# Kernel tuning notes

Measured on AMD Instinct MI355X. Metric: run time of the kernel, lower is better.

The kernel has to match this reference:

```python
import jax, jax.numpy as jnp
import numpy as np

KH, KW = 3, 3  # window_size[1], window_size[2]
SH, SW = 1, 1  # strides
FILTERS = 64


def _extract_patches(x, kh, kw, sh, sw):
    # TF tf.image.extract_patches ordering: depth = (row, col, channel), channel fastest.
    B, H, W, C = x.shape
    Ho = (H - kh) // sh + 1
    Wo = (W - kw) // sw + 1
    # stack kh*kw shifted views -> (B, Ho, Wo, kh*kw, C)
    views = [x[:, i:i + (Ho - 1) * sh + 1:sh, j:j + (Wo - 1) * sw + 1:sw, :]
             for i in range(kh) for j in range(kw)]
    patches = jnp.stack(views, axis=3)
    return patches.reshape(B, Ho, Wo, kh * kw * C)


def setup_inputs() -> dict:
    key = jax.random.key(0)
    k1, k2 = jax.random.split(key)
    B, H, W, C = 8, 32, 32, 32
    K = KH * KW * C  # 288
    x = jax.random.normal(k1, (B, H, W, C), dtype=jnp.float32)
    w = jax.random.normal(k2, (1, 1, 1, K, FILTERS), dtype=jnp.float32) * 0.05
    bias = jnp.zeros((FILTERS,), dtype=jnp.float32)
    return {"x": x, "w": w, "bias": bias}


def reference(x, w, bias):
    # patches: (B, Ho, Wo, K)
    patches = _extract_patches(x, KH, KW, SH, SW)
    # broadcast add: (B, Ho, Wo, K, F)
    s = patches[..., None] + w
    # tropical max-plus minus min-plus over the patch axis, plus bias
    return jnp.max(s, axis=3) - jnp.min(s, axis=3) + bias
```

## Files before the change

kernel.cpp:

```cpp
#include <hip/hip_runtime.h>
#include <math.h>


#define PIX 6

__global__ __launch_bounds__(64) void trop_kernel(
    const float* __restrict__ x,
    const float* __restrict__ w,
    const float* __restrict__ bias,
    float* __restrict__ out)
{
    const int lane = threadIdx.x;
    const int gid  = blockIdx.x;
    const int chunk = gid % 5;
    const int rowid = gid / 5;
    const int ho = rowid % 30;
    const int b  = rowid / 30;
    const int wo0 = chunk * PIX;

    const float* xbase = x + (((b * 32 + ho) * 32) + wo0) * 32;

    float amax[PIX], amin[PIX];
#pragma unroll
    for (int p = 0; p < PIX; ++p) {
        amax[p] = -INFINITY;
        amin[p] =  INFINITY;
    }

#pragma unroll
    for (int dydx = 0; dydx < 9; ++dydx) {
        const int dy = dydx / 3;
        const int dx = dydx % 3;
        const float* xp = xbase + (dy * 32 + dx) * 32;
        const float* wp = w + dydx * 32 * 64 + lane;

        for (int c = 0; c < 32; c += 4) {
            const float w0 = wp[(c + 0) * 64];
            const float w1 = wp[(c + 1) * 64];
            const float w2 = wp[(c + 2) * 64];
            const float w3 = wp[(c + 3) * 64];
#pragma unroll
            for (int p = 0; p < PIX; ++p) {
                const float4 xv = *(const float4*)(xp + p * 32 + c);
                const float s0 = xv.x + w0;
                const float s1 = xv.y + w1;
                const float s2 = xv.z + w2;
                const float s3 = xv.w + w3;
                amax[p] = fmaxf(fmaxf(fmaxf(fmaxf(amax[p], s0), s1), s2), s3);
                amin[p] = fminf(fminf(fminf(fminf(amin[p], s0), s1), s2), s3);
            }
        }
    }

    const float bv = bias[lane];
    float* op = out + (((b * 30 + ho) * 30) + wo0) * 64 + lane;
#pragma unroll
    for (int p = 0; p < PIX; ++p)
        op[p * 64] = amax[p] - amin[p] + bv;
}

extern "C" void kernel_launch(void* const* d_in, const int* in_sizes, int n_in,
                              void* d_out, int out_size, void* d_ws, size_t ws_size,
                              hipStream_t stream) {
    const float* x    = (const float*)d_in[0];
    const float* w    = (const float*)d_in[1];
    const float* bias = (const float*)d_in[2];
    float* out = (float*)d_out;

    trop_kernel<<<dim3(1200), dim3(64), 0, stream>>>(x, w, bias, out);
}
```

Measured before the change: 82.23 us.

## Stage weights in double-buffered LDS and shrink per-wave pixel tile

Weights for each 3x3 tap are cooperatively loaded into a double-buffered shared-memory tile by a 256-thread block. The next tap is prefetched into registers while the current one is used, so lanes no longer issue global loads for weights. The pixel tile per wave drops from 6 to 2, which raises the wave count (900 blocks of 4 waves) to improve latency hiding. The cost is a barrier per tap, extra LDS traffic, and less reuse of each weight value across pixels.

```diff
diff --git a/kernel.cpp b/kernel.cpp
--- a/kernel.cpp
+++ b/kernel.cpp
@@ -2,46 +2,68 @@
 #include <math.h>
 
 
-#define PIX 6
+#define PIX 2
+#define TPB 256
 
-__global__ __launch_bounds__(64) void trop_kernel(
+__global__ __launch_bounds__(TPB) void trop_kernel(
     const float* __restrict__ x,
     const float* __restrict__ w,
     const float* __restrict__ bias,
     float* __restrict__ out)
 {
-    const int lane = threadIdx.x;
-    const int gid  = blockIdx.x;
-    const int chunk = gid % 5;
-    const int rowid = gid / 5;
-    const int ho = rowid % 30;
-    const int b  = rowid / 30;
-    const int wo0 = chunk * PIX;
+    __shared__ float wlds[2][32 * 64];
 
-    const float* xbase = x + (((b * 32 + ho) * 32) + wo0) * 32;
+    const int tid  = threadIdx.x;
+    const int lane = tid & 63;
+    const int wv   = tid >> 6;
+
+    const int pix0 = blockIdx.x * (4 * PIX) + wv * PIX;
+
+    const float* xp[PIX];
+#pragma unroll
+    for (int p = 0; p < PIX; ++p) {
+        const int pid = pix0 + p;
+        const int wo = pid % 30;
+        const int t  = pid / 30;
+        const int ho = t % 30;
+        const int b  = t / 30;
+        xp[p] = x + (((b * 32 + ho) * 32) + wo) * 32;
+    }
 
     float amax[PIX], amin[PIX];
 #pragma unroll
-    for (int p = 0; p < PIX; ++p) {
-        amax[p] = -INFINITY;
-        amin[p] =  INFINITY;
+    for (int p = 0; p < PIX; ++p) { amax[p] = -INFINITY; amin[p] = INFINITY; }
+
+    {
+        const float4* src = (const float4*)w;
+        ((float4*)wlds[0])[tid]       = src[tid];
+        ((float4*)wlds[0])[tid + 256] = src[tid + 256];
     }
+    __syncthreads();
 
 #pragma unroll
-    for (int dydx = 0; dydx < 9; ++dydx) {
-        const int dy = dydx / 3;
-        const int dx = dydx % 3;
-        const float* xp = xbase + (dy * 32 + dx) * 32;
-        const float* wp = w + dydx * 32 * 64 + lane;
+    for (int tap = 0; tap < 9; ++tap) {
+        const int cur = tap & 1;
+        const int nxt = cur ^ 1;
 
+        const int ntap = (tap < 8) ? tap + 1 : 8;
+        const float4* src = (const float4*)(w + ntap * 2048);
+        const float4 r0 = src[tid];
+        const float4 r1 = src[tid + 256];
+
+        const int dy = tap / 3;
+        const int dx = tap % 3;
+        const int xoff = (dy * 32 + dx) * 32;
+
+#pragma unroll
         for (int c = 0; c < 32; c += 4) {
-            const float w0 = wp[(c + 0) * 64];
-            const float w1 = wp[(c + 1) * 64];
-            const float w2 = wp[(c + 2) * 64];
-            const float w3 = wp[(c + 3) * 64];
+            const float w0 = wlds[cur][(c + 0) * 64 + lane];
+            const float w1 = wlds[cur][(c + 1) * 64 + lane];
+            const float w2 = wlds[cur][(c + 2) * 64 + lane];
+            const float w3 = wlds[cur][(c + 3) * 64 + lane];
 #pragma unroll
             for (int p = 0; p < PIX; ++p) {
-                const float4 xv = *(const float4*)(xp + p * 32 + c);
+                const float4 xv = *(const float4*)(xp[p] + xoff + c);
                 const float s0 = xv.x + w0;
                 const float s1 = xv.y + w1;
                 const float s2 = xv.z + w2;
@@ -50,13 +72,16 @@
                 amin[p] = fminf(fminf(fminf(fminf(amin[p], s0), s1), s2), s3);
             }
         }
+
+        ((float4*)wlds[nxt])[tid]       = r0;
+        ((float4*)wlds[nxt])[tid + 256] = r1;
+        __syncthreads();
     }
 
     const float bv = bias[lane];
-    float* op = out + (((b * 30 + ho) * 30) + wo0) * 64 + lane;
 #pragma unroll
     for (int p = 0; p < PIX; ++p)
-        op[p * 64] = amax[p] - amin[p] + bv;
+        out[(pix0 + p) * 64 + lane] = amax[p] - amin[p] + bv;
 }
 
 extern "C" void kernel_launch(void* const* d_in, const int* in_sizes, int n_in,
@@ -67,5 +92,5 @@
     const float* bias = (const float*)d_in[2];
     float* out = (float*)d_out;
 
-    trop_kernel<<<dim3(1200), dim3(64), 0, stream>>>(x, w, bias, out);
+    trop_kernel<<<dim3(900), dim3(TPB), 0, stream>>>(x, w, bias, out);
 }
```

After: 77.79 us. 5.4% less time.
